# Optimization experiments

Hardware: AMD Instinct MI355X
Metric: run time of the kernel (lower is better)

## Reference

```python
import jax, jax.numpy as jnp
import numpy as np

B, S, E = 2, 2048, 2048
HQ, HK, D = 32, 8, 64
G = HQ // HK  # GQA groups

def _rope(t, cos, sin):
    # t: [B,S,H,D]; cos/sin: [1,S,1,D/2]
    t1, t2 = jnp.split(t, 2, axis=-1)
    return jnp.concatenate([t1 * cos - t2 * sin, t2 * cos + t1 * sin], axis=-1)

def setup_inputs() -> dict:
    key = jax.random.key(0)
    ks = jax.random.split(key, 8)
    sc = 1.0 / np.sqrt(E)
    return {
        "x": jax.random.normal(ks[0], (B, S, E), jnp.float32),
        "rope_cos": jax.random.uniform(ks[1], (1, S, 1, D // 2), jnp.float32),
        "rope_sin": jax.random.uniform(ks[2], (1, S, 1, D // 2), jnp.float32),
        "attn_mask": jnp.zeros((1, 1, S, S), jnp.float32),
        "Wq": jax.random.normal(ks[3], (E, HQ, D), jnp.float32) * sc,
        "Wk": jax.random.normal(ks[4], (E, HK, D), jnp.float32) * sc,
        "Wv": jax.random.normal(ks[5], (E, HK, D), jnp.float32) * sc,
        "Wo": jax.random.normal(ks[6], (HQ, D, E), jnp.float32) * (1.0 / np.sqrt(HQ * D)),
    }

def reference(x, rope_cos, rope_sin, attn_mask, Wq, Wk, Wv, Wo):
    # QKV projections (LinearGeneral, no bias)
    q = jnp.einsum('bse,ehd->bshd', x, Wq)
    k = jnp.einsum('bse,ehd->bshd', x, Wk)
    v = jnp.einsum('bse,ehd->bshd', x, Wv)
    # inline RoPE on q and k
    q = _rope(q, rope_cos, rope_sin)
    k = _rope(k, rope_cos, rope_sin)
    # [B,H,S,D]
    q = jnp.transpose(q, (0, 2, 1, 3))
    k = jnp.transpose(k, (0, 2, 1, 3))
    v = jnp.transpose(v, (0, 2, 1, 3))
    # GQA repeat of k/v to full query-head count (faithful to jnp.repeat in source)
    k = jnp.repeat(k, G, axis=1)
    v = jnp.repeat(v, G, axis=1)
    # explicit scores (NOTE: source applies no 1/sqrt(d) scaling)
    w = jnp.einsum('bhqd,bhkd->bhqk', q, k) + attn_mask
    w = jax.nn.softmax(w, axis=-1)
    o = jnp.einsum('bhqk,bhkd->bhqd', w, v)
    o = jnp.transpose(o, (0, 2, 1, 3))  # [B,S,H,D]
    return jnp.einsum('bshd,hde->bse', o, Wo)
```

## Files before the change

kernel.cpp:

```cpp
#include <hip/hip_runtime.h>
#include <hip/hip_bf16.h>

typedef __bf16 bf16_t;
typedef __bf16 bfrag __attribute__((ext_vector_type(8)));
typedef float f4 __attribute__((ext_vector_type(4)));

#define S_LEN 2048
#define HQ_N 32
#define HK_N 8
#define D_DIM 64
#define LOG2E 1.4426950408889634f

__global__ __launch_bounds__(256) void cvt_bf16(
    const float* __restrict__ src, bf16_t* __restrict__ dst, int n)
{
    int i = (blockIdx.x * 256 + threadIdx.x) * 8;
    if (i >= n) return;
    f4 a = *(const f4*)(src + i);
    f4 b = *(const f4*)(src + i + 4);
    bf16_t o[8];
#pragma unroll
    for (int j = 0; j < 4; ++j) { o[j] = (bf16_t)a[j]; o[4 + j] = (bf16_t)b[j]; }
    *(uint4*)(dst + i) = *(uint4*)o;
}

__global__ __launch_bounds__(256) void transpose_cvt(
    const float* __restrict__ src, bf16_t* __restrict__ dst,
    int K, int N, int row_off)
{
    __shared__ float T[32][33];
    const int n0 = blockIdx.x * 32;
    const int k0 = blockIdx.y * 32;
    const int tx = threadIdx.x;
    const int ty = threadIdx.y;
#pragma unroll
    for (int i = 0; i < 4; ++i)
        T[ty + 8 * i][tx] = src[(size_t)(k0 + ty + 8 * i) * N + n0 + tx];
    __syncthreads();
#pragma unroll
    for (int i = 0; i < 4; ++i)
        dst[(size_t)(row_off + n0 + ty + 8 * i) * K + k0 + tx] =
            (bf16_t)T[tx][ty + 8 * i];
}

template<bool OUT_BF16>
__global__ __launch_bounds__(256) void gemm_bt(
    const bf16_t* __restrict__ A, const bf16_t* __restrict__ Bt,
    void* __restrict__ Cv, int M, int N, int K, int ldc)
{
    __shared__ bf16_t As[128][72];
    __shared__ bf16_t Bs[128][72];
    const int tid  = threadIdx.x;
    const int wave = tid >> 6;
    const int lane = tid & 63;
    const int lrow = lane & 15;
    const int quad = lane >> 4;
    const int wm   = (wave >> 1) * 64;
    const int wn   = (wave & 1) * 64;
    const int bm   = blockIdx.y * 128;
    const int bn   = blockIdx.x * 128;

    f4 acc[4][4];
#pragma unroll
    for (int i = 0; i < 4; ++i)
#pragma unroll
        for (int j = 0; j < 4; ++j)
            acc[i][j] = (f4){0.f, 0.f, 0.f, 0.f};

    const int sr = tid >> 2;
    const int sc = (tid & 3) * 16;

    for (int k0 = 0; k0 < K; k0 += 64) {
        uint4 a0 = *(const uint4*)(A  + (size_t)(bm + sr)      * K + k0 + sc);
        uint4 a1 = *(const uint4*)(A  + (size_t)(bm + sr)      * K + k0 + sc + 8);
        uint4 a2 = *(const uint4*)(A  + (size_t)(bm + sr + 64) * K + k0 + sc);
        uint4 a3 = *(const uint4*)(A  + (size_t)(bm + sr + 64) * K + k0 + sc + 8);
        uint4 b0 = *(const uint4*)(Bt + (size_t)(bn + sr)      * K + k0 + sc);
        uint4 b1 = *(const uint4*)(Bt + (size_t)(bn + sr)      * K + k0 + sc + 8);
        uint4 b2 = *(const uint4*)(Bt + (size_t)(bn + sr + 64) * K + k0 + sc);
        uint4 b3 = *(const uint4*)(Bt + (size_t)(bn + sr + 64) * K + k0 + sc + 8);
        __syncthreads();
        *(uint4*)(&As[sr][sc])          = a0;
        *(uint4*)(&As[sr][sc + 8])      = a1;
        *(uint4*)(&As[sr + 64][sc])     = a2;
        *(uint4*)(&As[sr + 64][sc + 8]) = a3;
        *(uint4*)(&Bs[sr][sc])          = b0;
        *(uint4*)(&Bs[sr][sc + 8])      = b1;
        *(uint4*)(&Bs[sr + 64][sc])     = b2;
        *(uint4*)(&Bs[sr + 64][sc + 8]) = b3;
        __syncthreads();

#pragma unroll
        for (int kc = 0; kc < 2; ++kc) {
            bfrag aF[4], bF[4];
#pragma unroll
            for (int i = 0; i < 4; ++i)
                aF[i] = *(const bfrag*)(&As[wm + i * 16 + lrow][kc * 32 + quad * 8]);
#pragma unroll
            for (int j = 0; j < 4; ++j)
                bF[j] = *(const bfrag*)(&Bs[wn + j * 16 + lrow][kc * 32 + quad * 8]);
#pragma unroll
            for (int i = 0; i < 4; ++i)
#pragma unroll
                for (int j = 0; j < 4; ++j)
                    acc[i][j] = __builtin_amdgcn_mfma_f32_16x16x32_bf16(
                        aF[i], bF[j], acc[i][j], 0, 0, 0);
        }
    }

#pragma unroll
    for (int i = 0; i < 4; ++i)
#pragma unroll
        for (int j = 0; j < 4; ++j)
#pragma unroll
            for (int r = 0; r < 4; ++r) {
                int row = bm + wm + i * 16 + quad * 4 + r;
                int col = bn + wn + j * 16 + lrow;
                if (OUT_BF16)
                    ((bf16_t*)Cv)[(size_t)row * ldc + col] = (bf16_t)acc[i][j][r];
                else
                    ((float*)Cv)[(size_t)row * ldc + col] = acc[i][j][r];
            }
}

__global__ __launch_bounds__(256) void rope_fused(
    bf16_t* __restrict__ t, const float* __restrict__ cs,
    const float* __restrict__ sn)
{
    int idx = blockIdx.x * 256 + threadIdx.x;
    int cidx = idx % 1280;
    int row  = idx / 1280;
    int s    = row & (S_LEN - 1);
    int col, d1;
    float scale;
    if (cidx < 1024) {
        d1 = cidx & 31;
        col = (cidx >> 5) * 64 + d1;
        scale = LOG2E;
    } else {
        int c2 = cidx - 1024;
        d1 = c2 & 31;
        col = 2048 + (c2 >> 5) * 64 + d1;
        scale = 1.0f;
    }
    size_t base = (size_t)row * 3072 + col;
    float t1 = (float)t[base];
    float t2 = (float)t[base + 32];
    float c  = cs[s * 32 + d1];
    float s_ = sn[s * 32 + d1];
    t[base]      = (bf16_t)((t1 * c - t2 * s_) * scale);
    t[base + 32] = (bf16_t)((t2 * c + t1 * s_) * scale);
}

__global__ __launch_bounds__(256) void attn_mfma(
    const bf16_t* __restrict__ qkv, const float* __restrict__ mask,
    bf16_t* __restrict__ o)
{
    __shared__ bf16_t Ks[64][72];
    __shared__ bf16_t Vt[64][72];
    __shared__ bf16_t Ps[128][72];

    const int tid  = threadIdx.x;
    const int wave = tid >> 6;
    const int lane = tid & 63;
    const int lrow = lane & 15;
    const int quad = lane >> 4;
    const int qt   = blockIdx.x;
    const int h    = blockIdx.y;
    const int b    = blockIdx.z;
    const int hk   = h >> 2;
    const int s0   = qt * 128;
    const int wrow = wave * 32;

    bfrag vOnes;
#pragma unroll
    for (int j = 0; j < 8; ++j) vOnes[j] = (lrow == 0) ? (bf16_t)1.0f : (bf16_t)0.0f;

    bfrag qf[2][2];
#pragma unroll
    for (int m = 0; m < 2; ++m) {
        const bf16_t* qsrc = qkv + (size_t)(b * S_LEN + s0 + wrow + m * 16 + lrow) * 3072 + h * 64;
#pragma unroll
        for (int c = 0; c < 2; ++c)
            qf[m][c] = *(const bfrag*)(qsrc + c * 32 + quad * 8);
    }

    f4 oacc[2][4], lacc[2];
#pragma unroll
    for (int m = 0; m < 2; ++m) {
        lacc[m] = (f4){0.f, 0.f, 0.f, 0.f};
#pragma unroll
        for (int n = 0; n < 4; ++n) oacc[m][n] = (f4){0.f, 0.f, 0.f, 0.f};
    }

    const int skey = tid >> 2;
    const int sdc  = (tid & 3) * 16;
    const int vg   = tid >> 5;
    const int vp   = tid & 31;

    for (int kt = 0; kt < 32; ++kt) {
        const bf16_t* ksrc = qkv + (size_t)(b * S_LEN + kt * 64 + skey) * 3072 + 2048 + hk * 64 + sdc;
        uint4 k0 = *(const uint4*)(ksrc);
        uint4 k1 = *(const uint4*)(ksrc + 8);
        unsigned int vw[8];
#pragma unroll
        for (int kk = 0; kk < 8; ++kk)
            vw[kk] = *(const unsigned int*)(qkv + (size_t)(b * S_LEN + kt * 64 + vg * 8 + kk) * 3072
                                            + 2560 + hk * 64 + 2 * vp);
        __syncthreads();
        *(uint4*)(&Ks[skey][sdc])     = k0;
        *(uint4*)(&Ks[skey][sdc + 8]) = k1;
        {
            unsigned short lo[8], hi[8];
#pragma unroll
            for (int kk = 0; kk < 8; ++kk) { lo[kk] = vw[kk] & 0xffff; hi[kk] = vw[kk] >> 16; }
            *(uint4*)(&Vt[2 * vp][vg * 8])     = *(uint4*)lo;
            *(uint4*)(&Vt[2 * vp + 1][vg * 8]) = *(uint4*)hi;
        }
        __syncthreads();

        float mk[2][4][4];
#pragma unroll
        for (int m = 0; m < 2; ++m)
#pragma unroll
            for (int n = 0; n < 4; ++n)
#pragma unroll
                for (int r = 0; r < 4; ++r)
                    mk[m][n][r] = mask[(size_t)(s0 + wrow + m * 16 + quad * 4 + r) * S_LEN
                                       + kt * 64 + n * 16 + lrow];

        bfrag kf[4][2];
#pragma unroll
        for (int n = 0; n < 4; ++n)
#pragma unroll
            for (int c = 0; c < 2; ++c)
                kf[n][c] = *(const bfrag*)(&Ks[n * 16 + lrow][c * 32 + quad * 8]);

        f4 sc[2][4];
#pragma unroll
        for (int m = 0; m < 2; ++m)
#pragma unroll
            for (int n = 0; n < 4; ++n) {
                f4 a = (f4){0.f, 0.f, 0.f, 0.f};
                a = __builtin_amdgcn_mfma_f32_16x16x32_bf16(qf[m][0], kf[n][0], a, 0, 0, 0);
                a = __builtin_amdgcn_mfma_f32_16x16x32_bf16(qf[m][1], kf[n][1], a, 0, 0, 0);
                sc[m][n] = a;
            }

#pragma unroll
        for (int m = 0; m < 2; ++m)
#pragma unroll
            for (int n = 0; n < 4; ++n)
#pragma unroll
                for (int r = 0; r < 4; ++r) {
                    float p = exp2f(fmaf(mk[m][n][r], LOG2E, sc[m][n][r]));
                    Ps[wrow + m * 16 + quad * 4 + r][n * 16 + lrow] = (bf16_t)p;
                }

        bfrag pf[2][2], vf[4][2];
#pragma unroll
        for (int m = 0; m < 2; ++m)
#pragma unroll
            for (int c = 0; c < 2; ++c)
                pf[m][c] = *(const bfrag*)(&Ps[wrow + m * 16 + lrow][c * 32 + quad * 8]);
#pragma unroll
        for (int n = 0; n < 4; ++n)
#pragma unroll
            for (int c = 0; c < 2; ++c)
                vf[n][c] = *(const bfrag*)(&Vt[n * 16 + lrow][c * 32 + quad * 8]);
#pragma unroll
        for (int m = 0; m < 2; ++m) {
#pragma unroll
            for (int n = 0; n < 4; ++n) {
                oacc[m][n] = __builtin_amdgcn_mfma_f32_16x16x32_bf16(pf[m][0], vf[n][0], oacc[m][n], 0, 0, 0);
                oacc[m][n] = __builtin_amdgcn_mfma_f32_16x16x32_bf16(pf[m][1], vf[n][1], oacc[m][n], 0, 0, 0);
            }
            lacc[m] = __builtin_amdgcn_mfma_f32_16x16x32_bf16(pf[m][0], vOnes, lacc[m], 0, 0, 0);
            lacc[m] = __builtin_amdgcn_mfma_f32_16x16x32_bf16(pf[m][1], vOnes, lacc[m], 0, 0, 0);
        }
    }

#pragma unroll
    for (int m = 0; m < 2; ++m)
#pragma unroll
        for (int r = 0; r < 4; ++r) {
            float lv = __shfl(lacc[m][r], lane & 48, 64);
            float inv = 1.f / lv;
            int row = b * S_LEN + s0 + wrow + m * 16 + quad * 4 + r;
#pragma unroll
            for (int n = 0; n < 4; ++n)
                o[(size_t)row * 2048 + h * 64 + n * 16 + lrow] = (bf16_t)(oacc[m][n][r] * inv);
        }
}

extern "C" void kernel_launch(void* const* d_in, const int* in_sizes, int n_in,
                              void* d_out, int out_size, void* d_ws, size_t ws_size,
                              hipStream_t stream)
{
    const float* x    = (const float*)d_in[0];
    const float* rc   = (const float*)d_in[1];
    const float* rs   = (const float*)d_in[2];
    const float* mask = (const float*)d_in[3];
    const float* Wq   = (const float*)d_in[4];
    const float* Wk   = (const float*)d_in[5];
    const float* Wv   = (const float*)d_in[6];
    const float* Wo   = (const float*)d_in[7];
    float* out = (float*)d_out;

    char* ws = (char*)d_ws;
    bf16_t* qkv = (bf16_t*)(ws);
    bf16_t* xb  = (bf16_t*)(ws + (24u << 20));
    bf16_t* ob  = xb;
    bf16_t* Wt3 = (bf16_t*)(ws + (40u << 20));
    bf16_t* Wot = (bf16_t*)(ws + (52u << 20));

    const int M = 2 * S_LEN;
    dim3 blk(256);

    cvt_bf16<<<(M * 2048) / (256 * 8), blk, 0, stream>>>(x, xb, M * 2048);
    transpose_cvt<<<dim3(64, 64), dim3(32, 8), 0, stream>>>(Wq, Wt3, 2048, 2048, 0);
    transpose_cvt<<<dim3(16, 64), dim3(32, 8), 0, stream>>>(Wk, Wt3, 2048,  512, 2048);
    transpose_cvt<<<dim3(16, 64), dim3(32, 8), 0, stream>>>(Wv, Wt3, 2048,  512, 2560);
    transpose_cvt<<<dim3(64, 64), dim3(32, 8), 0, stream>>>(Wo, Wot, 2048, 2048, 0);

    gemm_bt<true><<<dim3(3072 / 128, M / 128), blk, 0, stream>>>(
        xb, Wt3, qkv, M, 3072, 2048, 3072);

    rope_fused<<<(M * 1280) / 256, blk, 0, stream>>>(qkv, rc, rs);

    attn_mfma<<<dim3(16, 32, 2), blk, 0, stream>>>(qkv, mask, ob);

    gemm_bt<false><<<dim3(2048 / 128, M / 128), blk, 0, stream>>>(
        ob, Wot, out, M, 2048, 2048, 2048);
}
```

Before: 425.1 us.

## Use direct global-to-LDS loads with XOR swizzle in GEMM; transpose attention MFMA operands

The GEMM now stages A and B tiles with global_load_lds straight into unpadded, XOR-swizzled shared memory, which removes the register round trip and the padding. The fragment reads apply the same swizzle. The attention kernel swaps MFMA operand order so each lane holds four consecutive keys per query row. That allows vectorized float4 mask loads, packed uint2 stores of P and packed output stores. The changes add risk in swizzle correctness and in how synchronization interacts with the asynchronous LDS loads.

```diff
diff --git a/kernel.cpp b/kernel.cpp
--- a/kernel.cpp
+++ b/kernel.cpp
@@ -11,6 +11,10 @@
 #define D_DIM 64
 #define LOG2E 1.4426950408889634f
 
+#define GLDS16(gp, lp) __builtin_amdgcn_global_load_lds( \
+    (const __attribute__((address_space(1))) void*)(gp), \
+    (__attribute__((address_space(3))) void*)(lp), 16, 0, 0)
+
 __global__ __launch_bounds__(256) void cvt_bf16(
     const float* __restrict__ src, bf16_t* __restrict__ dst, int n)
 {
@@ -48,8 +52,8 @@
     const bf16_t* __restrict__ A, const bf16_t* __restrict__ Bt,
     void* __restrict__ Cv, int M, int N, int K, int ldc)
 {
-    __shared__ bf16_t As[128][72];
-    __shared__ bf16_t Bs[128][72];
+    __shared__ bf16_t As[128][64];
+    __shared__ bf16_t Bs[128][64];
     const int tid  = threadIdx.x;
     const int wave = tid >> 6;
     const int lane = tid & 63;
@@ -60,6 +64,12 @@
     const int bm   = blockIdx.y * 128;
     const int bn   = blockIdx.x * 128;
 
+    const int glr = lane >> 3;
+    const int glc = (lane & 7) ^ glr;
+
+    const bf16_t* Ab = A  + (size_t)(bm + glr) * K + glc * 8;
+    const bf16_t* Bb = Bt + (size_t)(bn + glr) * K + glc * 8;
+
     f4 acc[4][4];
 #pragma unroll
     for (int i = 0; i < 4; ++i)
@@ -67,27 +77,14 @@
         for (int j = 0; j < 4; ++j)
             acc[i][j] = (f4){0.f, 0.f, 0.f, 0.f};
 
-    const int sr = tid >> 2;
-    const int sc = (tid & 3) * 16;
-
     for (int k0 = 0; k0 < K; k0 += 64) {
-        uint4 a0 = *(const uint4*)(A  + (size_t)(bm + sr)      * K + k0 + sc);
-        uint4 a1 = *(const uint4*)(A  + (size_t)(bm + sr)      * K + k0 + sc + 8);
-        uint4 a2 = *(const uint4*)(A  + (size_t)(bm + sr + 64) * K + k0 + sc);
-        uint4 a3 = *(const uint4*)(A  + (size_t)(bm + sr + 64) * K + k0 + sc + 8);
-        uint4 b0 = *(const uint4*)(Bt + (size_t)(bn + sr)      * K + k0 + sc);
-        uint4 b1 = *(const uint4*)(Bt + (size_t)(bn + sr)      * K + k0 + sc + 8);
-        uint4 b2 = *(const uint4*)(Bt + (size_t)(bn + sr + 64) * K + k0 + sc);
-        uint4 b3 = *(const uint4*)(Bt + (size_t)(bn + sr + 64) * K + k0 + sc + 8);
         __syncthreads();
-        *(uint4*)(&As[sr][sc])          = a0;
-        *(uint4*)(&As[sr][sc + 8])      = a1;
-        *(uint4*)(&As[sr + 64][sc])     = a2;
-        *(uint4*)(&As[sr + 64][sc + 8]) = a3;
-        *(uint4*)(&Bs[sr][sc])          = b0;
-        *(uint4*)(&Bs[sr][sc + 8])      = b1;
-        *(uint4*)(&Bs[sr + 64][sc])     = b2;
-        *(uint4*)(&Bs[sr + 64][sc + 8]) = b3;
+#pragma unroll
+        for (int t = 0; t < 4; ++t) {
+            const int rb = wave * 8 + t * 32;
+            GLDS16(Ab + (size_t)rb * K + k0, &As[rb][0]);
+            GLDS16(Bb + (size_t)rb * K + k0, &Bs[rb][0]);
+        }
         __syncthreads();
 
 #pragma unroll
@@ -95,10 +92,12 @@
             bfrag aF[4], bF[4];
 #pragma unroll
             for (int i = 0; i < 4; ++i)
-                aF[i] = *(const bfrag*)(&As[wm + i * 16 + lrow][kc * 32 + quad * 8]);
+                aF[i] = *(const bfrag*)(&As[wm + i * 16 + lrow]
+                                           [(((kc << 2) + quad) ^ (lrow & 7)) * 8]);
 #pragma unroll
             for (int j = 0; j < 4; ++j)
-                bF[j] = *(const bfrag*)(&Bs[wn + j * 16 + lrow][kc * 32 + quad * 8]);
+                bF[j] = *(const bfrag*)(&Bs[wn + j * 16 + lrow]
+                                           [(((kc << 2) + quad) ^ (lrow & 7)) * 8]);
 #pragma unroll
             for (int i = 0; i < 4; ++i)
 #pragma unroll
@@ -172,25 +171,25 @@
     const int s0   = qt * 128;
     const int wrow = wave * 32;
 
-    bfrag vOnes;
-#pragma unroll
-    for (int j = 0; j < 8; ++j) vOnes[j] = (lrow == 0) ? (bf16_t)1.0f : (bf16_t)0.0f;
+    bfrag aOnes;
+#pragma unroll
+    for (int j = 0; j < 8; ++j) aOnes[j] = (lrow == 0) ? (bf16_t)1.0f : (bf16_t)0.0f;
 
     bfrag qf[2][2];
 #pragma unroll
-    for (int m = 0; m < 2; ++m) {
-        const bf16_t* qsrc = qkv + (size_t)(b * S_LEN + s0 + wrow + m * 16 + lrow) * 3072 + h * 64;
-#pragma unroll
-        for (int c = 0; c < 2; ++c)
-            qf[m][c] = *(const bfrag*)(qsrc + c * 32 + quad * 8);
-    }
-
-    f4 oacc[2][4], lacc[2];
-#pragma unroll
-    for (int m = 0; m < 2; ++m) {
-        lacc[m] = (f4){0.f, 0.f, 0.f, 0.f};
-#pragma unroll
-        for (int n = 0; n < 4; ++n) oacc[m][n] = (f4){0.f, 0.f, 0.f, 0.f};
+    for (int nt = 0; nt < 2; ++nt) {
+        const bf16_t* qsrc = qkv + (size_t)(b * S_LEN + s0 + wrow + nt * 16 + lrow) * 3072 + h * 64;
+#pragma unroll
+        for (int kc = 0; kc < 2; ++kc)
+            qf[nt][kc] = *(const bfrag*)(qsrc + kc * 32 + quad * 8);
+    }
+
+    f4 oacc[4][2], lacc[2];
+#pragma unroll
+    for (int nt = 0; nt < 2; ++nt) {
+        lacc[nt] = (f4){0.f, 0.f, 0.f, 0.f};
+#pragma unroll
+        for (int dt = 0; dt < 4; ++dt) oacc[dt][nt] = (f4){0.f, 0.f, 0.f, 0.f};
     }
 
     const int skey = tid >> 2;
@@ -200,16 +199,16 @@
 
     for (int kt = 0; kt < 32; ++kt) {
         const bf16_t* ksrc = qkv + (size_t)(b * S_LEN + kt * 64 + skey) * 3072 + 2048 + hk * 64 + sdc;
-        uint4 k0 = *(const uint4*)(ksrc);
-        uint4 k1 = *(const uint4*)(ksrc + 8);
+        uint4 k0v = *(const uint4*)(ksrc);
+        uint4 k1v = *(const uint4*)(ksrc + 8);
         unsigned int vw[8];
 #pragma unroll
         for (int kk = 0; kk < 8; ++kk)
             vw[kk] = *(const unsigned int*)(qkv + (size_t)(b * S_LEN + kt * 64 + vg * 8 + kk) * 3072
                                             + 2560 + hk * 64 + 2 * vp);
         __syncthreads();
-        *(uint4*)(&Ks[skey][sdc])     = k0;
-        *(uint4*)(&Ks[skey][sdc + 8]) = k1;
+        *(uint4*)(&Ks[skey][sdc])     = k0v;
+        *(uint4*)(&Ks[skey][sdc + 8]) = k1v;
         {
             unsigned short lo[8], hi[8];
 #pragma unroll
@@ -219,78 +218,80 @@
         }
         __syncthreads();
 
-        float mk[2][4][4];
-#pragma unroll
-        for (int m = 0; m < 2; ++m)
-#pragma unroll
-            for (int n = 0; n < 4; ++n)
+        f4 mk[2][4];
+#pragma unroll
+        for (int nt = 0; nt < 2; ++nt)
+#pragma unroll
+            for (int mt = 0; mt < 4; ++mt)
+                mk[nt][mt] = *(const f4*)(mask
+                    + (size_t)(s0 + wrow + nt * 16 + lrow) * S_LEN
+                    + kt * 64 + mt * 16 + quad * 4);
+
+        bfrag kf[4][2];
+#pragma unroll
+        for (int mt = 0; mt < 4; ++mt)
+#pragma unroll
+            for (int kc = 0; kc < 2; ++kc)
+                kf[mt][kc] = *(const bfrag*)(&Ks[mt * 16 + lrow][kc * 32 + quad * 8]);
+
+        f4 sc[4][2];
+#pragma unroll
+        for (int mt = 0; mt < 4; ++mt)
+#pragma unroll
+            for (int nt = 0; nt < 2; ++nt) {
+                f4 a = (f4){0.f, 0.f, 0.f, 0.f};
+                a = __builtin_amdgcn_mfma_f32_16x16x32_bf16(kf[mt][0], qf[nt][0], a, 0, 0, 0);
+                a = __builtin_amdgcn_mfma_f32_16x16x32_bf16(kf[mt][1], qf[nt][1], a, 0, 0, 0);
+                sc[mt][nt] = a;
+            }
+
+#pragma unroll
+        for (int nt = 0; nt < 2; ++nt)
+#pragma unroll
+            for (int mt = 0; mt < 4; ++mt) {
+                bf16_t pp[4];
 #pragma unroll
                 for (int r = 0; r < 4; ++r)
-                    mk[m][n][r] = mask[(size_t)(s0 + wrow + m * 16 + quad * 4 + r) * S_LEN
-                                       + kt * 64 + n * 16 + lrow];
-
-        bfrag kf[4][2];
-#pragma unroll
-        for (int n = 0; n < 4; ++n)
-#pragma unroll
-            for (int c = 0; c < 2; ++c)
-                kf[n][c] = *(const bfrag*)(&Ks[n * 16 + lrow][c * 32 + quad * 8]);
-
-        f4 sc[2][4];
-#pragma unroll
-        for (int m = 0; m < 2; ++m)
-#pragma unroll
-            for (int n = 0; n < 4; ++n) {
-                f4 a = (f4){0.f, 0.f, 0.f, 0.f};
-                a = __builtin_amdgcn_mfma_f32_16x16x32_bf16(qf[m][0], kf[n][0], a, 0, 0, 0);
-                a = __builtin_amdgcn_mfma_f32_16x16x32_bf16(qf[m][1], kf[n][1], a, 0, 0, 0);
-                sc[m][n] = a;
+                    pp[r] = (bf16_t)exp2f(fmaf(mk[nt][mt][r], LOG2E, sc[mt][nt][r]));
+                *(uint2*)(&Ps[wrow + nt * 16 + lrow][mt * 16 + quad * 4]) = *(uint2*)pp;
             }
 
-#pragma unroll
-        for (int m = 0; m < 2; ++m)
-#pragma unroll
-            for (int n = 0; n < 4; ++n)
-#pragma unroll
-                for (int r = 0; r < 4; ++r) {
-                    float p = exp2f(fmaf(mk[m][n][r], LOG2E, sc[m][n][r]));
-                    Ps[wrow + m * 16 + quad * 4 + r][n * 16 + lrow] = (bf16_t)p;
-                }
-
         bfrag pf[2][2], vf[4][2];
 #pragma unroll
-        for (int m = 0; m < 2; ++m)
-#pragma unroll
-            for (int c = 0; c < 2; ++c)
-                pf[m][c] = *(const bfrag*)(&Ps[wrow + m * 16 + lrow][c * 32 + quad * 8]);
-#pragma unroll
-        for (int n = 0; n < 4; ++n)
-#pragma unroll
-            for (int c = 0; c < 2; ++c)
-                vf[n][c] = *(const bfrag*)(&Vt[n * 16 + lrow][c * 32 + quad * 8]);
-#pragma unroll
-        for (int m = 0; m < 2; ++m) {
-#pragma unroll
-            for (int n = 0; n < 4; ++n) {
-                oacc[m][n] = __builtin_amdgcn_mfma_f32_16x16x32_bf16(pf[m][0], vf[n][0], oacc[m][n], 0, 0, 0);
-                oacc[m][n] = __builtin_amdgcn_mfma_f32_16x16x32_bf16(pf[m][1], vf[n][1], oacc[m][n], 0, 0, 0);
+        for (int nt = 0; nt < 2; ++nt)
+#pragma unroll
+            for (int kc = 0; kc < 2; ++kc)
+                pf[nt][kc] = *(const bfrag*)(&Ps[wrow + nt * 16 + lrow][kc * 32 + quad * 8]);
+#pragma unroll
+        for (int dt = 0; dt < 4; ++dt)
+#pragma unroll
+            for (int kc = 0; kc < 2; ++kc)
+                vf[dt][kc] = *(const bfrag*)(&Vt[dt * 16 + lrow][kc * 32 + quad * 8]);
+#pragma unroll
+        for (int nt = 0; nt < 2; ++nt) {
+#pragma unroll
+            for (int dt = 0; dt < 4; ++dt) {
+                oacc[dt][nt] = __builtin_amdgcn_mfma_f32_16x16x32_bf16(vf[dt][0], pf[nt][0], oacc[dt][nt], 0, 0, 0);
+                oacc[dt][nt] = __builtin_amdgcn_mfma_f32_16x16x32_bf16(vf[dt][1], pf[nt][1], oacc[dt][nt], 0, 0, 0);
             }
-            lacc[m] = __builtin_amdgcn_mfma_f32_16x16x32_bf16(pf[m][0], vOnes, lacc[m], 0, 0, 0);
-            lacc[m] = __builtin_amdgcn_mfma_f32_16x16x32_bf16(pf[m][1], vOnes, lacc[m], 0, 0, 0);
-        }
-    }
-
-#pragma unroll
-    for (int m = 0; m < 2; ++m)
-#pragma unroll
-        for (int r = 0; r < 4; ++r) {
-            float lv = __shfl(lacc[m][r], lane & 48, 64);
-            float inv = 1.f / lv;
-            int row = b * S_LEN + s0 + wrow + m * 16 + quad * 4 + r;
-#pragma unroll
-            for (int n = 0; n < 4; ++n)
-                o[(size_t)row * 2048 + h * 64 + n * 16 + lrow] = (bf16_t)(oacc[m][n][r] * inv);
-        }
+            lacc[nt] = __builtin_amdgcn_mfma_f32_16x16x32_bf16(aOnes, pf[nt][0], lacc[nt], 0, 0, 0);
+            lacc[nt] = __builtin_amdgcn_mfma_f32_16x16x32_bf16(aOnes, pf[nt][1], lacc[nt], 0, 0, 0);
+        }
+    }
+
+#pragma unroll
+    for (int nt = 0; nt < 2; ++nt) {
+        float lv  = __shfl(lacc[nt][0], lrow, 64);
+        float inv = 1.f / lv;
+        size_t rowb = (size_t)(b * S_LEN + s0 + wrow + nt * 16 + lrow) * 2048 + h * 64;
+#pragma unroll
+        for (int dt = 0; dt < 4; ++dt) {
+            bf16_t ov[4];
+#pragma unroll
+            for (int r = 0; r < 4; ++r) ov[r] = (bf16_t)(oacc[dt][nt][r] * inv);
+            *(uint2*)(o + rowb + dt * 16 + quad * 4) = *(uint2*)ov;
+        }
+    }
 }
 
 extern "C" void kernel_launch(void* const* d_in, const int* in_sizes, int n_in,
```

Measured after the change: 440.1 us. 1.04x slower.

## Use direct global-to-LDS loads with XOR swizzle in GEMM and prefetch K/V in attention

Applied to the files above, without the earlier changes.

The GEMM tile loads now go through global_load_lds, which writes global data straight into LDS without a register round trip. The padded LDS rows become unpadded 64-wide rows, and an XOR swizzle on the 16-byte chunk index avoids bank conflicts. The attention kernel register-prefetches the next K/V tile while the current one is computed, and adds a minimum-occupancy hint to launch bounds. This hides global load latency and cuts VGPR staging, at the cost of more live registers in attention and reliance on correct swizzle indexing.

```diff
diff --git a/kernel.cpp b/kernel.cpp
--- a/kernel.cpp
+++ b/kernel.cpp
@@ -11,6 +11,10 @@
 #define D_DIM 64
 #define LOG2E 1.4426950408889634f
 
+#define GLDS16(gp, lp) __builtin_amdgcn_global_load_lds( \
+    (const __attribute__((address_space(1))) void*)(gp), \
+    (__attribute__((address_space(3))) void*)(lp), 16, 0, 0)
+
 __global__ __launch_bounds__(256) void cvt_bf16(
     const float* __restrict__ src, bf16_t* __restrict__ dst, int n)
 {
@@ -48,8 +52,8 @@
     const bf16_t* __restrict__ A, const bf16_t* __restrict__ Bt,
     void* __restrict__ Cv, int M, int N, int K, int ldc)
 {
-    __shared__ bf16_t As[128][72];
-    __shared__ bf16_t Bs[128][72];
+    __shared__ bf16_t As[128][64];
+    __shared__ bf16_t Bs[128][64];
     const int tid  = threadIdx.x;
     const int wave = tid >> 6;
     const int lane = tid & 63;
@@ -60,6 +64,12 @@
     const int bm   = blockIdx.y * 128;
     const int bn   = blockIdx.x * 128;
 
+    const int glr = lane >> 3;
+    const int glc = (lane & 7) ^ glr;
+
+    const bf16_t* Ab = A  + (size_t)(bm + glr) * K + glc * 8;
+    const bf16_t* Bb = Bt + (size_t)(bn + glr) * K + glc * 8;
+
     f4 acc[4][4];
 #pragma unroll
     for (int i = 0; i < 4; ++i)
@@ -67,27 +77,14 @@
         for (int j = 0; j < 4; ++j)
             acc[i][j] = (f4){0.f, 0.f, 0.f, 0.f};
 
-    const int sr = tid >> 2;
-    const int sc = (tid & 3) * 16;
-
     for (int k0 = 0; k0 < K; k0 += 64) {
-        uint4 a0 = *(const uint4*)(A  + (size_t)(bm + sr)      * K + k0 + sc);
-        uint4 a1 = *(const uint4*)(A  + (size_t)(bm + sr)      * K + k0 + sc + 8);
-        uint4 a2 = *(const uint4*)(A  + (size_t)(bm + sr + 64) * K + k0 + sc);
-        uint4 a3 = *(const uint4*)(A  + (size_t)(bm + sr + 64) * K + k0 + sc + 8);
-        uint4 b0 = *(const uint4*)(Bt + (size_t)(bn + sr)      * K + k0 + sc);
-        uint4 b1 = *(const uint4*)(Bt + (size_t)(bn + sr)      * K + k0 + sc + 8);
-        uint4 b2 = *(const uint4*)(Bt + (size_t)(bn + sr + 64) * K + k0 + sc);
-        uint4 b3 = *(const uint4*)(Bt + (size_t)(bn + sr + 64) * K + k0 + sc + 8);
         __syncthreads();
-        *(uint4*)(&As[sr][sc])          = a0;
-        *(uint4*)(&As[sr][sc + 8])      = a1;
-        *(uint4*)(&As[sr + 64][sc])     = a2;
-        *(uint4*)(&As[sr + 64][sc + 8]) = a3;
-        *(uint4*)(&Bs[sr][sc])          = b0;
-        *(uint4*)(&Bs[sr][sc + 8])      = b1;
-        *(uint4*)(&Bs[sr + 64][sc])     = b2;
-        *(uint4*)(&Bs[sr + 64][sc + 8]) = b3;
+#pragma unroll
+        for (int t = 0; t < 4; ++t) {
+            const int rb = wave * 8 + t * 32;
+            GLDS16(Ab + (size_t)rb * K + k0, &As[rb][0]);
+            GLDS16(Bb + (size_t)rb * K + k0, &Bs[rb][0]);
+        }
         __syncthreads();
 
 #pragma unroll
@@ -95,10 +92,12 @@
             bfrag aF[4], bF[4];
 #pragma unroll
             for (int i = 0; i < 4; ++i)
-                aF[i] = *(const bfrag*)(&As[wm + i * 16 + lrow][kc * 32 + quad * 8]);
+                aF[i] = *(const bfrag*)(&As[wm + i * 16 + lrow]
+                                           [(((kc << 2) + quad) ^ (lrow & 7)) * 8]);
 #pragma unroll
             for (int j = 0; j < 4; ++j)
-                bF[j] = *(const bfrag*)(&Bs[wn + j * 16 + lrow][kc * 32 + quad * 8]);
+                bF[j] = *(const bfrag*)(&Bs[wn + j * 16 + lrow]
+                                           [(((kc << 2) + quad) ^ (lrow & 7)) * 8]);
 #pragma unroll
             for (int i = 0; i < 4; ++i)
 #pragma unroll
@@ -152,7 +151,7 @@
     t[base + 32] = (bf16_t)((t2 * c + t1 * s_) * scale);
 }
 
-__global__ __launch_bounds__(256) void attn_mfma(
+__global__ __launch_bounds__(256, 4) void attn_mfma(
     const bf16_t* __restrict__ qkv, const float* __restrict__ mask,
     bf16_t* __restrict__ o)
 {
@@ -198,18 +197,23 @@
     const int vg   = tid >> 5;
     const int vp   = tid & 31;
 
+    const bf16_t* kvb = qkv + (size_t)(b * S_LEN) * 3072 + 2048 + hk * 64;
+
+    uint4 kr0, kr1;
+    unsigned int vw[8];
+    {
+        const bf16_t* ksrc = kvb + (size_t)skey * 3072 + sdc;
+        kr0 = *(const uint4*)(ksrc);
+        kr1 = *(const uint4*)(ksrc + 8);
+#pragma unroll
+        for (int kk = 0; kk < 8; ++kk)
+            vw[kk] = *(const unsigned int*)(kvb + 512 + (size_t)(vg * 8 + kk) * 3072 + 2 * vp);
+    }
+
     for (int kt = 0; kt < 32; ++kt) {
-        const bf16_t* ksrc = qkv + (size_t)(b * S_LEN + kt * 64 + skey) * 3072 + 2048 + hk * 64 + sdc;
-        uint4 k0 = *(const uint4*)(ksrc);
-        uint4 k1 = *(const uint4*)(ksrc + 8);
-        unsigned int vw[8];
-#pragma unroll
-        for (int kk = 0; kk < 8; ++kk)
-            vw[kk] = *(const unsigned int*)(qkv + (size_t)(b * S_LEN + kt * 64 + vg * 8 + kk) * 3072
-                                            + 2560 + hk * 64 + 2 * vp);
         __syncthreads();
-        *(uint4*)(&Ks[skey][sdc])     = k0;
-        *(uint4*)(&Ks[skey][sdc + 8]) = k1;
+        *(uint4*)(&Ks[skey][sdc])     = kr0;
+        *(uint4*)(&Ks[skey][sdc + 8]) = kr1;
         {
             unsigned short lo[8], hi[8];
 #pragma unroll
@@ -218,6 +222,17 @@
             *(uint4*)(&Vt[2 * vp + 1][vg * 8]) = *(uint4*)hi;
         }
         __syncthreads();
+
+        {
+            const int ktn = (kt < 31) ? kt + 1 : 31;
+            const bf16_t* ksrc = kvb + (size_t)(ktn * 64 + skey) * 3072 + sdc;
+            kr0 = *(const uint4*)(ksrc);
+            kr1 = *(const uint4*)(ksrc + 8);
+#pragma unroll
+            for (int kk = 0; kk < 8; ++kk)
+                vw[kk] = *(const unsigned int*)(kvb + 512
+                         + (size_t)(ktn * 64 + vg * 8 + kk) * 3072 + 2 * vp);
+        }
 
         float mk[2][4][4];
 #pragma unroll
```

Result: slower. 519.1 us (+22.1%).
